# Kernel optimization log

Hardware: AMD Instinct MI355X
Metric: run time of the kernel (lower is better)

Reference implementation:

```python
import jax, jax.numpy as jnp
import numpy as np

HIDDEN = 2048
N_HEADS = 16
HEAD_DIM = HIDDEN // N_HEADS  # 128
GROUP_SIZE = 128
ROPE_THETA = 10000.0
EPS = 1e-8
THRESH = 0.5


def ternary_quantize_groupwise(w):
    O, I = w.shape
    wg = w.reshape(O, I // GROUP_SIZE, GROUP_SIZE)
    scale = jnp.maximum(jnp.mean(jnp.abs(wg), axis=-1, keepdims=True), EPS)
    wn = wg / scale
    q = jnp.where(wn > THRESH, 1.0, jnp.where(wn < -THRESH, -1.0, 0.0))
    return (q * scale).reshape(O, I)


def quantize_with_ste(w):
    wq = ternary_quantize_groupwise(w)
    return w + jax.lax.stop_gradient(wq - w)


def rope_tables(seqlen):
    half = HEAD_DIM // 2
    inv_freq = 1.0 / (ROPE_THETA ** (jnp.arange(half, dtype=jnp.float32) / half))
    freqs = jnp.arange(seqlen, dtype=jnp.float32)[:, None] * inv_freq[None, :]  # [S, half]
    return jnp.cos(freqs), jnp.sin(freqs)


def apply_rope(x, cos, sin):
    # x: [B, H, S, D]; cos/sin: [S, D/2]
    d = x.shape[-1]
    x1, x2 = x[..., : d // 2], x[..., d // 2:]
    c = cos[None, None, :, :].astype(x.dtype)
    s = sin[None, None, :, :].astype(x.dtype)
    return jnp.concatenate([x1 * c - x2 * s, x1 * s + x2 * c], axis=-1)


def setup_inputs() -> dict:
    key = jax.random.key(0)
    ks = jax.random.split(key, 5)
    B, S = 1, 2048
    hidden_states = jax.random.normal(ks[0], (B, S, HIDDEN), dtype=jnp.float32)
    attention_mask = jnp.ones((B, S), dtype=jnp.int32)
    init_scale = 1.0 / np.sqrt(HIDDEN)
    wq = jax.random.normal(ks[1], (HIDDEN, HIDDEN), dtype=jnp.float32) * init_scale
    wk = jax.random.normal(ks[2], (HIDDEN, HIDDEN), dtype=jnp.float32) * init_scale
    wv = jax.random.normal(ks[3], (HIDDEN, HIDDEN), dtype=jnp.float32) * init_scale
    wo = jax.random.normal(ks[4], (HIDDEN, HIDDEN), dtype=jnp.float32) * init_scale
    return {"hidden_states": hidden_states, "attention_mask": attention_mask,
            "wq": wq, "wk": wk, "wv": wv, "wo": wo}


def reference(hidden_states, attention_mask, wq, wk, wv, wo):
    B, S, _ = hidden_states.shape
    cos, sin = rope_tables(S)

    def proj(x, w):
        w_q = quantize_with_ste(w)
        y = jnp.einsum('bsi,oi->bso', x, w_q)
        return y.reshape(B, S, N_HEADS, HEAD_DIM).transpose(0, 2, 1, 3)  # [B,H,S,D]

    q = apply_rope(proj(hidden_states, wq), cos, sin)
    k = apply_rope(proj(hidden_states, wk), cos, sin)
    v = proj(hidden_states, wv)

    scores = jnp.einsum('bhsd,bhtd->bhst', q, k) / np.sqrt(HEAD_DIM)
    causal = jnp.triu(jnp.ones((S, S), dtype=bool), k=1)
    scores = jnp.where(causal[None, None, :, :], -jnp.inf, scores)
    pad = (attention_mask == 0)[:, None, None, :]
    scores = jnp.where(pad, -jnp.inf, scores)

    probs = jax.nn.softmax(scores, axis=-1)
    out = jnp.einsum('bhst,bhtd->bhsd', probs, v)
    out = out.transpose(0, 2, 1, 3).reshape(B, S, HIDDEN)

    wo_q = quantize_with_ste(wo)
    return jnp.einsum('bso,po->bsp', out, wo_q)
```

## Files before the change

### kernel.cpp

```cpp
#include <hip/hip_runtime.h>
#include <cstdint>
#include <cstddef>


typedef __attribute__((ext_vector_type(8))) short bf16x8;
typedef __attribute__((ext_vector_type(4))) float f32x4;
typedef __attribute__((address_space(3))) void lds_void;
typedef const __attribute__((address_space(1))) void gmem_void;

__device__ __forceinline__ short f2bf(float x) {
    union { float f; uint32_t u; } c; c.f = x;
    uint32_t r = (c.u + 0x7FFFu + ((c.u >> 16) & 1u)) >> 16;
    return (short)r;
}
__device__ __forceinline__ float bf2f(short x) {
    union { uint32_t u; float f; } c; c.u = ((uint32_t)(uint16_t)x) << 16;
    return c.f;
}

__global__ __launch_bounds__(64) void zero_flag(int* f) {
    if (threadIdx.x == 0) *f = 0;
}

__global__ __launch_bounds__(256) void detect_kernel(
    const unsigned short* __restrict__ p, int n, int* __restrict__ flag)
{
    int tid = blockIdx.x * 256 + threadIdx.x;
    int cnt = 0;
    for (int i = tid; i < n; i += 65536) {
        int e = (p[i] >> 7) & 0xFF;
        cnt += (e >= 0xF0) ? 1 : 0;
    }
#pragma unroll
    for (int off = 1; off < 64; off <<= 1) cnt += __shfl_xor(cnt, off);
    if ((threadIdx.x & 63) == 0 && cnt) atomicAdd(flag, cnt);
}

__global__ __launch_bounds__(256) void convert_kernel(
    const void* __restrict__ in, short* __restrict__ out, int n,
    const int* __restrict__ flag)
{
    bool isf32 = (*flag > 1000);
    int i = (blockIdx.x * 256 + threadIdx.x) * 4;
    if (i >= n) return;
    if (isf32) {
        float4 v = *(const float4*)((const float*)in + i);
        short4 o;
        o.x = f2bf(v.x); o.y = f2bf(v.y); o.z = f2bf(v.z); o.w = f2bf(v.w);
        *(short4*)(out + i) = o;
    } else {
        *(short4*)(out + i) = *(const short4*)((const short*)in + i);
    }
}

__global__ __launch_bounds__(256) void quant_kernel(
    const void* __restrict__ w0, const void* __restrict__ w1,
    const void* __restrict__ w2, const void* __restrict__ w3,
    short* __restrict__ q0, short* __restrict__ q1,
    short* __restrict__ q2, short* __restrict__ q3,
    const int* __restrict__ flag)
{
    bool isf32 = (*flag > 1000);
    int t   = blockIdx.x * 256 + threadIdx.x;
    int mat = t >> 20;
    int e4  = t & 1048575;
    const void* w = (mat == 0) ? w0 : (mat == 1) ? w1 : (mat == 2) ? w2 : w3;
    short*      q = (mat == 0) ? q0 : (mat == 1) ? q1 : (mat == 2) ? q2 : q3;
    float a0, a1, a2, a3;
    if (isf32) {
        float4 v = *(const float4*)((const float*)w + (long long)e4 * 4);
        a0 = v.x; a1 = v.y; a2 = v.z; a3 = v.w;
    } else {
        short4 v = *(const short4*)((const short*)w + (long long)e4 * 4);
        a0 = bf2f(v.x); a1 = bf2f(v.y); a2 = bf2f(v.z); a3 = bf2f(v.w);
    }
    float s = fabsf(a0) + fabsf(a1) + fabsf(a2) + fabsf(a3);
#pragma unroll
    for (int off = 1; off < 32; off <<= 1) s += __shfl_xor(s, off);
    float scale = fmaxf(s * (1.0f / 128.0f), 1e-8f);
    float inv = 1.0f / scale;
    auto qz = [&](float a) -> short {
        float na = a * inv;
        return f2bf((na > 0.5f) ? scale : (na < -0.5f) ? -scale : 0.0f);
    };
    short4 o;
    o.x = qz(a0); o.y = qz(a1); o.z = qz(a2); o.w = qz(a3);
    *(short4*)(q + (long long)e4 * 4) = o;
}

__global__ __launch_bounds__(256, 2) void gemm_qkv(
    const short* __restrict__ A, const short* __restrict__ B,
    short* __restrict__ C)
{
    __shared__ short lds[30720];

    int wg = blockIdx.y * 32 + blockIdx.x;
    int sw = (wg & 7) * 64 + (wg >> 3);
    int bx = sw & 31, by = sw >> 5;

    const short* Ab = A + (long long)by * 128 * 2048;
    const short* Bb = B + (long long)bx * 192 * 2048;

    int tid = threadIdx.x, lane = tid & 63, wid = tid >> 6;
    int wr = wid >> 1, wc = wid & 1;
    int quad = lane >> 4, lm = lane & 15;

    f32x4 acc[4][6];
#pragma unroll
    for (int i = 0; i < 4; i++)
#pragma unroll
        for (int j = 0; j < 6; j++)
#pragma unroll
            for (int r = 0; r < 4; r++) acc[i][j][r] = 0.0f;

    auto stage = [&](int tn, short* buf) {
        short* dA = buf;
        short* dB = buf + 4096;
#pragma unroll
        for (int l = 0; l < 2; l++) {
            int ci  = l * 256 + tid;
            int row = ci >> 2;
            int kc  = ((ci & 3) - (row >> 1)) & 3;
            const short* gp = Ab + (long long)row * 2048 + tn * 32 + kc * 8;
            __builtin_amdgcn_global_load_lds((gmem_void*)gp, (lds_void*)(dA + ci * 8), 16, 0, 0);
        }
#pragma unroll
        for (int l = 0; l < 3; l++) {
            int ci  = l * 256 + tid;
            int row = ci >> 2;
            int kc  = ((ci & 3) - (row >> 1)) & 3;
            const short* gp = Bb + (long long)row * 2048 + tn * 32 + kc * 8;
            __builtin_amdgcn_global_load_lds((gmem_void*)gp, (lds_void*)(dB + ci * 8), 16, 0, 0);
        }
    };

    auto tile = [&](short* cur, short* nxt, int tn, bool pf) {
        if (pf) stage(tn, nxt);
        short* cA = cur;
        short* cB = cur + 4096;
        bf16x8 af[4], bg[6];
#pragma unroll
        for (int m = 0; m < 4; m++) {
            int R = wr * 64 + m * 16 + lm;
            af[m] = *(const bf16x8*)(cA + R * 32 + (((quad + (R >> 1)) & 3) << 3));
        }
#pragma unroll
        for (int n = 0; n < 3; n++) {
            int R = wc * 96 + n * 16 + lm;
            bg[n] = *(const bf16x8*)(cB + R * 32 + (((quad + (R >> 1)) & 3) << 3));
        }
        __builtin_amdgcn_s_setprio(1);
#pragma unroll
        for (int m = 0; m < 4; m++)
#pragma unroll
            for (int n = 0; n < 3; n++)
                acc[m][n] = __builtin_amdgcn_mfma_f32_16x16x32_bf16(af[m], bg[n], acc[m][n], 0, 0, 0);
        __builtin_amdgcn_s_setprio(0);
#pragma unroll
        for (int n = 3; n < 6; n++) {
            int R = wc * 96 + n * 16 + lm;
            bg[n] = *(const bf16x8*)(cB + R * 32 + (((quad + (R >> 1)) & 3) << 3));
        }
        __builtin_amdgcn_s_setprio(1);
#pragma unroll
        for (int m = 0; m < 4; m++)
#pragma unroll
            for (int n = 3; n < 6; n++)
                acc[m][n] = __builtin_amdgcn_mfma_f32_16x16x32_bf16(af[m], bg[n], acc[m][n], 0, 0, 0);
        __builtin_amdgcn_s_setprio(0);
        if (pf) asm volatile("s_waitcnt vmcnt(5)" ::: "memory");
        else    asm volatile("s_waitcnt vmcnt(0)" ::: "memory");
        __builtin_amdgcn_s_barrier();
    };

    short* c0 = lds;
    short* c1 = lds + 10240;
    short* c2 = lds + 20480;
    stage(0, c0);
    stage(1, c1);
    asm volatile("s_waitcnt vmcnt(5)" ::: "memory");
    __builtin_amdgcn_s_barrier();

    for (int t = 0; t < 64; t++) {
        tile(c0, c2, t + 2, t + 2 < 64);
        short* tmp = c0; c0 = c1; c1 = c2; c2 = tmp;
    }

#pragma unroll
    for (int m = 0; m < 4; m++)
#pragma unroll
        for (int n = 0; n < 6; n++)
#pragma unroll
            for (int r = 0; r < 4; r++) {
                int row = by * 128 + wr * 64 + m * 16 + quad * 4 + r;
                int col = bx * 192 + wc * 96 + n * 16 + lm;
                C[(long long)row * 6144 + col] = f2bf(acc[m][n][r]);
            }
}

__global__ __launch_bounds__(256) void vtrans_kernel(
    const short* __restrict__ qkv, short* __restrict__ v_t)
{
    __shared__ short lt[4096];
    int bt = blockIdx.x, bo = blockIdx.y;
    int tid = threadIdx.x;
    int r = tid >> 3, c = tid & 7;
#pragma unroll
    for (int h = 0; h < 2; h++) {
        int row = h * 32 + r;
        bf16x8 v = *(const bf16x8*)(qkv + (long long)(bt * 64 + row) * 6144 + 4096 + bo * 64 + c * 8);
        *(bf16x8*)(lt + row * 64 + ((c ^ (row & 7)) << 3)) = v;
    }
    __syncthreads();
#pragma unroll
    for (int h = 0; h < 2; h++) {
        int o = h * 32 + r;
        bf16x8 ov;
#pragma unroll
        for (int k = 0; k < 8; k++) {
            int row = c * 8 + k;
            ov[k] = lt[row * 64 + ((((o >> 3) ^ (row & 7))) << 3) + (o & 7)];
        }
        *(bf16x8*)(v_t + (long long)(bo * 64 + o) * 2048 + bt * 64 + c * 8) = ov;
    }
}

__global__ __launch_bounds__(256, 2) void gemm_wo(
    const short* __restrict__ A, const short* __restrict__ B,
    float* __restrict__ C)
{
    __shared__ short lds[18432];

    int wg = blockIdx.y * 32 + blockIdx.x;
    int sw = (wg & 7) * 64 + (wg >> 3);
    int bx = sw & 31, by = sw >> 5;

    const short* Ab = A + (long long)by * 128 * 2048;
    const short* Bb = B + (long long)bx * 64 * 2048;

    int tid = threadIdx.x, lane = tid & 63, wid = tid >> 6;
    int wr = wid >> 1, wc = wid & 1;
    int quad = lane >> 4, lm = lane & 15;

    f32x4 acc[4][2];
#pragma unroll
    for (int i = 0; i < 4; i++)
#pragma unroll
        for (int j = 0; j < 2; j++)
#pragma unroll
            for (int r = 0; r < 4; r++) acc[i][j][r] = 0.0f;

    auto stage = [&](int tn, short* buf) {
        short* dA = buf;
        short* dB = buf + 4096;
#pragma unroll
        for (int l = 0; l < 2; l++) {
            int ci  = l * 256 + tid;
            int row = ci >> 2;
            int kc  = ((ci & 3) - (row >> 1)) & 3;
            const short* gp = Ab + (long long)row * 2048 + tn * 32 + kc * 8;
            __builtin_amdgcn_global_load_lds((gmem_void*)gp, (lds_void*)(dA + ci * 8), 16, 0, 0);
        }
        {
            int ci  = tid;
            int row = ci >> 2;
            int kc  = ((ci & 3) - (row >> 1)) & 3;
            const short* gp = Bb + (long long)row * 2048 + tn * 32 + kc * 8;
            __builtin_amdgcn_global_load_lds((gmem_void*)gp, (lds_void*)(dB + ci * 8), 16, 0, 0);
        }
    };

    auto tile = [&](short* cur, short* nxt, int tn, bool pf) {
        if (pf) stage(tn, nxt);
        short* cA = cur;
        short* cB = cur + 4096;
        bf16x8 af[4], bg[2];
#pragma unroll
        for (int m = 0; m < 4; m++) {
            int R = wr * 64 + m * 16 + lm;
            af[m] = *(const bf16x8*)(cA + R * 32 + (((quad + (R >> 1)) & 3) << 3));
        }
#pragma unroll
        for (int n = 0; n < 2; n++) {
            int R = wc * 32 + n * 16 + lm;
            bg[n] = *(const bf16x8*)(cB + R * 32 + (((quad + (R >> 1)) & 3) << 3));
        }
        __builtin_amdgcn_s_setprio(1);
#pragma unroll
        for (int m = 0; m < 4; m++)
#pragma unroll
            for (int n = 0; n < 2; n++)
                acc[m][n] = __builtin_amdgcn_mfma_f32_16x16x32_bf16(af[m], bg[n], acc[m][n], 0, 0, 0);
        __builtin_amdgcn_s_setprio(0);
        if (pf) asm volatile("s_waitcnt vmcnt(3)" ::: "memory");
        else    asm volatile("s_waitcnt vmcnt(0)" ::: "memory");
        __builtin_amdgcn_s_barrier();
    };

    short* c0 = lds;
    short* c1 = lds + 6144;
    short* c2 = lds + 12288;
    stage(0, c0);
    stage(1, c1);
    asm volatile("s_waitcnt vmcnt(3)" ::: "memory");
    __builtin_amdgcn_s_barrier();

    for (int t = 0; t < 64; t++) {
        tile(c0, c2, t + 2, t + 2 < 64);
        short* tmp = c0; c0 = c1; c1 = c2; c2 = tmp;
    }

#pragma unroll
    for (int m = 0; m < 4; m++)
#pragma unroll
        for (int n = 0; n < 2; n++)
#pragma unroll
            for (int r = 0; r < 4; r++) {
                int row = by * 128 + wr * 64 + m * 16 + quad * 4 + r;
                int col = bx * 64 + wc * 32 + n * 16 + lm;
                C[(long long)row * 2048 + col] = acc[m][n][r];
            }
}

__global__ __launch_bounds__(256) void rope_kernel(
    const short* __restrict__ qk,
    short* __restrict__ qr, short* __restrict__ kr)
{
    const float QSC = 0.1275174150637756f;
    int idx = blockIdx.x * 256 + threadIdx.x;
    int d8 = (idx & 7) * 8;
    int h  = (idx >> 3) & 15;
    int s  = idx >> 7;
    long long io = (long long)s * 6144 + h * 128 + d8;
    long long oo = (long long)h * 262144 + (long long)s * 128 + d8;
    bf16x8 x1q = *(const bf16x8*)(qk + io);
    bf16x8 x2q = *(const bf16x8*)(qk + io + 64);
    bf16x8 x1k = *(const bf16x8*)(qk + io + 2048);
    bf16x8 x2k = *(const bf16x8*)(qk + io + 2112);
    bf16x8 o1q, o2q, o1k, o2k;
#pragma unroll
    for (int j = 0; j < 8; j++) {
        float inv = exp2f((float)(d8 + j) * -0.20762050593261719f);
        float ang = (float)s * inv;
        float sn, c;
        sincosf(ang, &sn, &c);
        float a1 = bf2f(x1q[j]), a2 = bf2f(x2q[j]);
        o1q[j] = f2bf((a1 * c - a2 * sn) * QSC);
        o2q[j] = f2bf((a1 * sn + a2 * c) * QSC);
        float b1 = bf2f(x1k[j]), b2 = bf2f(x2k[j]);
        o1k[j] = f2bf(b1 * c - b2 * sn);
        o2k[j] = f2bf(b1 * sn + b2 * c);
    }
    *(bf16x8*)(qr + oo)      = o1q;
    *(bf16x8*)(qr + oo + 64) = o2q;
    *(bf16x8*)(kr + oo)      = o1k;
    *(bf16x8*)(kr + oo + 64) = o2k;
}

__global__ __launch_bounds__(256) void flash_kernel(
    const short* __restrict__ q_r, const short* __restrict__ k_r,
    const short* __restrict__ v_t, float* __restrict__ Opart,
    float* __restrict__ mpart, float* __restrict__ lpart)
{
    const float THR = 11.5f;
    int bid = blockIdx.x;
    int p = bid >> 5;
    int h = (bid >> 1) & 15;
    int z = bid & 1;

    int tid = threadIdx.x, lane = tid & 63, wv = tid >> 6;
    int quad = lane >> 4, lm = lane & 15;

    __shared__ short lK[64 * 128];
    __shared__ short lV[128 * 64];
    __shared__ short lP[64 * 64];

    const short* kb = k_r + h * 262144;
    const short* vb = v_t + h * 128 * 2048;

    for (int leg = 0; leg < 2; leg++) {
        int qt = leg ? p : 31 - p;
        int n  = qt + 1;
        int jhalf = (n + 1) >> 1;
        int jb = z ? jhalf : 0;
        int je = z ? n : jhalf;

        const short* qb = q_r + h * 262144 + (qt * 64 + wv * 16) * 128;
        bf16x8 aq[4];
#pragma unroll
        for (int kc = 0; kc < 4; kc++)
            aq[kc] = *(const bf16x8*)(qb + lm * 128 + kc * 32 + quad * 8);

        f32x4 ao[8];
#pragma unroll
        for (int nt = 0; nt < 8; nt++)
#pragma unroll
            for (int r = 0; r < 4; r++) ao[nt][r] = 0.0f;
        float mrow[4], lrow[4];
#pragma unroll
        for (int r = 0; r < 4; r++) { mrow[r] = -1e30f; lrow[r] = 0.0f; }

        if (jb < je) {
#pragma unroll
            for (int i = 0; i < 4; i++) {
                int ci = i * 256 + tid;
                int r = ci >> 4, cp = ci & 15;
                int c = (cp & 8) | ((cp & 7) ^ (r & 7));
                const short* gp = kb + (jb * 64 + r) * 128 + c * 8;
                __builtin_amdgcn_global_load_lds((gmem_void*)gp, (lds_void*)(lK + ci * 8), 16, 0, 0);
            }
        }
        __syncthreads();

        for (int jt = jb; jt < je; jt++) {
#pragma unroll
            for (int i = 0; i < 4; i++) {
                int ci = i * 256 + tid;
                int r = ci >> 3, cp = ci & 7;
                int c = cp ^ (r & 7);
                const short* gp = vb + r * 2048 + jt * 64 + c * 8;
                __builtin_amdgcn_global_load_lds((gmem_void*)gp, (lds_void*)(lV + ci * 8), 16, 0, 0);
            }
            f32x4 as[4];
#pragma unroll
            for (int nt = 0; nt < 4; nt++)
#pragma unroll
                for (int r = 0; r < 4; r++) as[nt][r] = 0.0f;
            __builtin_amdgcn_s_setprio(1);
#pragma unroll
            for (int kc = 0; kc < 4; kc++) {
#pragma unroll
                for (int nt = 0; nt < 4; nt++) {
                    int r = nt * 16 + lm;
                    int c = kc * 4 + quad;
                    int slot = (c & 8) | ((c & 7) ^ (r & 7));
                    bf16x8 bk = *(const bf16x8*)(lK + (r * 16 + slot) * 8);
                    as[nt] = __builtin_amdgcn_mfma_f32_16x16x32_bf16(aq[kc], bk, as[nt], 0, 0, 0);
                }
            }
            __builtin_amdgcn_s_setprio(0);
            if (jt == qt) {
#pragma unroll
                for (int nt = 0; nt < 4; nt++)
#pragma unroll
                    for (int r = 0; r < 4; r++) {
                        int qg = wv * 16 + quad * 4 + r;
                        int tg = nt * 16 + lm;
                        if (tg > qg) as[nt][r] = -1e30f;
                    }
            }
#pragma unroll
            for (int r = 0; r < 4; r++) {
                float lmax = fmaxf(fmaxf(as[0][r], as[1][r]), fmaxf(as[2][r], as[3][r]));
                if (__any(lmax > mrow[r] + THR)) {
                    float mx = lmax;
#pragma unroll
                    for (int off = 1; off < 16; off <<= 1) mx = fmaxf(mx, __shfl_xor(mx, off));
                    if (mx > mrow[r] + THR) {
                        float alpha = exp2f(mrow[r] - mx);
                        lrow[r] *= alpha;
#pragma unroll
                        for (int nt = 0; nt < 8; nt++) ao[nt][r] *= alpha;
                        mrow[r] = mx;
                    }
                }
                float ps = 0.0f;
#pragma unroll
                for (int nt = 0; nt < 4; nt++) {
                    float pv = exp2f(as[nt][r] - mrow[r]);
                    as[nt][r] = pv;
                    ps += pv;
                }
                lrow[r] += ps;
                int row = wv * 16 + quad * 4 + r;
#pragma unroll
                for (int nt = 0; nt < 4; nt++) {
                    int slot = (nt * 2 + (lm >> 3) + 2 * quad) & 7;
                    lP[row * 64 + slot * 8 + (lm & 7)] = f2bf(as[nt][r]);
                }
            }
            __syncthreads();
            if (jt + 1 < je) {
#pragma unroll
                for (int i = 0; i < 4; i++) {
                    int ci = i * 256 + tid;
                    int r = ci >> 4, cp = ci & 15;
                    int c = (cp & 8) | ((cp & 7) ^ (r & 7));
                    const short* gp = kb + ((jt + 1) * 64 + r) * 128 + c * 8;
                    __builtin_amdgcn_global_load_lds((gmem_void*)gp, (lds_void*)(lK + ci * 8), 16, 0, 0);
                }
            }
            __builtin_amdgcn_s_setprio(1);
#pragma unroll
            for (int kt = 0; kt < 2; kt++) {
                int prow = wv * 16 + lm;
                int slot = (kt * 4 + quad + 2 * (lm >> 2)) & 7;
                bf16x8 ap = *(const bf16x8*)(lP + prow * 64 + slot * 8);
#pragma unroll
                for (int nt = 0; nt < 8; nt++) {
                    int r = nt * 16 + lm;
                    int c = kt * 4 + quad;
                    int vslot = c ^ (r & 7);
                    bf16x8 bv = *(const bf16x8*)(lV + (r * 8 + vslot) * 8);
                    ao[nt] = __builtin_amdgcn_mfma_f32_16x16x32_bf16(ap, bv, ao[nt], 0, 0, 0);
                }
            }
            __builtin_amdgcn_s_setprio(0);
            __syncthreads();
        }

        float* Ob = Opart + (long long)z * 4194304;
#pragma unroll
        for (int r = 0; r < 4; r++) {
            float l = lrow[r];
#pragma unroll
            for (int off = 1; off < 16; off <<= 1) l += __shfl_xor(l, off);
            int sg = qt * 64 + wv * 16 + quad * 4 + r;
#pragma unroll
            for (int nt = 0; nt < 8; nt++) {
                int dg = h * 128 + nt * 16 + lm;
                Ob[(long long)sg * 2048 + dg] = ao[nt][r];
            }
            if (lm == 0) {
                mpart[z * 32768 + h * 2048 + sg] = mrow[r];
                lpart[z * 32768 + h * 2048 + sg] = l;
            }
        }
    }
}

__global__ __launch_bounds__(256) void combine_kernel(
    const float* __restrict__ O0, const float* __restrict__ O1,
    const float* __restrict__ mpart, const float* __restrict__ lpart,
    short* __restrict__ attn)
{
    int idx = blockIdx.x * 256 + threadIdx.x;
    int e = idx * 4;
    int s = e >> 11, h = (e & 2047) >> 7;
    float m0 = mpart[h * 2048 + s], m1 = mpart[32768 + h * 2048 + s];
    float l0 = lpart[h * 2048 + s], l1 = lpart[32768 + h * 2048 + s];
    float M = fmaxf(m0, m1);
    float w0 = exp2f(m0 - M), w1 = exp2f(m1 - M);
    float inv = 1.0f / (l0 * w0 + l1 * w1);
    float4 a = *(const float4*)(O0 + e);
    float4 b = *(const float4*)(O1 + e);
    short4 o;
    o.x = f2bf((a.x * w0 + b.x * w1) * inv);
    o.y = f2bf((a.y * w0 + b.y * w1) * inv);
    o.z = f2bf((a.z * w0 + b.z * w1) * inv);
    o.w = f2bf((a.w * w0 + b.w * w1) * inv);
    *(short4*)(attn + e) = o;
}

extern "C" void kernel_launch(void* const* d_in, const int* in_sizes, int n_in,
                              void* d_out, int out_size, void* d_ws, size_t ws_size,
                              hipStream_t stream)
{
    const void* x  = d_in[0];
    const void* wq = d_in[2];
    const void* wk = d_in[3];
    const void* wv = d_in[4];
    const void* wo = d_in[5];

    char* ws = (char*)d_ws;
    size_t off = 0;
    auto alloc = [&](size_t b) { void* p = ws + off; off += (b + 255) & ~(size_t)255; return p; };
    short* wqkv_q = (short*)alloc(25165824);
    short* wo_q   = (short*)alloc(8388608);
    float* Opart  = (float*)alloc(33554432);
    short* qkv    = (short*)Opart;
    short* v_t    = (short*)alloc(8388608);
    short* q_r    = (short*)alloc(8388608);
    short* k_r    = (short*)alloc(8388608);
    short* attn   = (short*)alloc(8388608);
    short* x_bf   = (short*)alloc(8388608);
    float* mpart  = (float*)alloc(262144);
    float* lpart  = (float*)alloc(262144);
    int*   flag   = (int*)alloc(256);
    if (off > ws_size) return;

    zero_flag<<<1, 64, 0, stream>>>(flag);
    detect_kernel<<<256, 256, 0, stream>>>(
        (const unsigned short*)x, in_sizes[0], flag);
    convert_kernel<<<4096, 256, 0, stream>>>(x, x_bf, 4194304, flag);

    quant_kernel<<<16384, 256, 0, stream>>>(wq, wk, wv, wo,
        wqkv_q, wqkv_q + 4194304, wqkv_q + 8388608, wo_q, flag);

    gemm_qkv<<<dim3(32, 16), 256, 0, stream>>>(x_bf, wqkv_q, qkv);

    rope_kernel<<<1024, 256, 0, stream>>>(qkv, q_r, k_r);
    vtrans_kernel<<<dim3(32, 32), 256, 0, stream>>>(qkv, v_t);

    flash_kernel<<<512, 256, 0, stream>>>(q_r, k_r, v_t, Opart, mpart, lpart);
    combine_kernel<<<4096, 256, 0, stream>>>(
        Opart, Opart + 4194304, mpart, lpart, attn);

    gemm_wo<<<dim3(32, 16), 256, 0, stream>>>(attn, wo_q, (float*)d_out);
}
```

Measured before the change: 306.1 us.

## Split flash attention KV range four ways and merge partials

Flash attention now splits each query tile's KV range into four chunks instead of two, doubling the grid to 1024 blocks, and sets a minimum occupancy of 4 blocks per CU. The combine kernel merges four partial outputs, skipping chunks that are empty. Partial buffers reuse dead workspace regions (the quantized QKV weights and the bf16 x scratch) to avoid extra allocation. The aim is better CU utilisation on the MI355X. In exchange it adds more partial-output write and read traffic, a heavier combine step, and register pressure from the occupancy bound.

```diff
diff --git a/kernel.cpp b/kernel.cpp
--- a/kernel.cpp
+++ b/kernel.cpp
@@ -357,16 +357,18 @@
     *(bf16x8*)(kr + oo + 64) = o2k;
 }
 
-__global__ __launch_bounds__(256) void flash_kernel(
+__global__ __launch_bounds__(256, 4) void flash_kernel(
     const short* __restrict__ q_r, const short* __restrict__ k_r,
-    const short* __restrict__ v_t, float* __restrict__ Opart,
+    const short* __restrict__ v_t,
+    float* __restrict__ O0, float* __restrict__ O1,
+    float* __restrict__ O2, float* __restrict__ O3,
     float* __restrict__ mpart, float* __restrict__ lpart)
 {
     const float THR = 11.5f;
     int bid = blockIdx.x;
-    int p = bid >> 5;
-    int h = (bid >> 1) & 15;
-    int z = bid & 1;
+    int zq = bid & 3;
+    int h  = (bid >> 2) & 15;
+    int p  = bid >> 6;
 
     int tid = threadIdx.x, lane = tid & 63, wv = tid >> 6;
     int quad = lane >> 4, lm = lane & 15;
@@ -377,13 +379,13 @@
 
     const short* kb = k_r + h * 262144;
     const short* vb = v_t + h * 128 * 2048;
+    float* Ob = (zq == 0) ? O0 : (zq == 1) ? O1 : (zq == 2) ? O2 : O3;
 
     for (int leg = 0; leg < 2; leg++) {
         int qt = leg ? p : 31 - p;
         int n  = qt + 1;
-        int jhalf = (n + 1) >> 1;
-        int jb = z ? jhalf : 0;
-        int je = z ? n : jhalf;
+        int jb = (n * zq) >> 2;
+        int je = (n * (zq + 1)) >> 2;
 
         const short* qb = q_r + h * 262144 + (qt * 64 + wv * 16) * 128;
         bf16x8 aq[4];
@@ -509,21 +511,22 @@
             __syncthreads();
         }
 
-        float* Ob = Opart + (long long)z * 4194304;
 #pragma unroll
         for (int r = 0; r < 4; r++) {
             float l = lrow[r];
 #pragma unroll
             for (int off = 1; off < 16; off <<= 1) l += __shfl_xor(l, off);
             int sg = qt * 64 + wv * 16 + quad * 4 + r;
-#pragma unroll
-            for (int nt = 0; nt < 8; nt++) {
-                int dg = h * 128 + nt * 16 + lm;
-                Ob[(long long)sg * 2048 + dg] = ao[nt][r];
+            if (jb < je) {
+#pragma unroll
+                for (int nt = 0; nt < 8; nt++) {
+                    int dg = h * 128 + nt * 16 + lm;
+                    Ob[(long long)sg * 2048 + dg] = ao[nt][r];
+                }
             }
             if (lm == 0) {
-                mpart[z * 32768 + h * 2048 + sg] = mrow[r];
-                lpart[z * 32768 + h * 2048 + sg] = l;
+                mpart[zq * 32768 + h * 2048 + sg] = mrow[r];
+                lpart[zq * 32768 + h * 2048 + sg] = l;
             }
         }
     }
@@ -531,24 +534,37 @@
 
 __global__ __launch_bounds__(256) void combine_kernel(
     const float* __restrict__ O0, const float* __restrict__ O1,
+    const float* __restrict__ O2, const float* __restrict__ O3,
     const float* __restrict__ mpart, const float* __restrict__ lpart,
     short* __restrict__ attn)
 {
     int idx = blockIdx.x * 256 + threadIdx.x;
     int e = idx * 4;
     int s = e >> 11, h = (e & 2047) >> 7;
-    float m0 = mpart[h * 2048 + s], m1 = mpart[32768 + h * 2048 + s];
-    float l0 = lpart[h * 2048 + s], l1 = lpart[32768 + h * 2048 + s];
-    float M = fmaxf(m0, m1);
-    float w0 = exp2f(m0 - M), w1 = exp2f(m1 - M);
-    float inv = 1.0f / (l0 * w0 + l1 * w1);
-    float4 a = *(const float4*)(O0 + e);
-    float4 b = *(const float4*)(O1 + e);
+    float m[4], l[4];
+#pragma unroll
+    for (int i = 0; i < 4; i++) {
+        m[i] = mpart[i * 32768 + h * 2048 + s];
+        l[i] = lpart[i * 32768 + h * 2048 + s];
+    }
+    float M = fmaxf(fmaxf(m[0], m[1]), fmaxf(m[2], m[3]));
+    const float* Os[4] = { O0, O1, O2, O3 };
+    float den = 0.0f, ax = 0.0f, ay = 0.0f, az = 0.0f, aw = 0.0f;
+#pragma unroll
+    for (int i = 0; i < 4; i++) {
+        if (l[i] > 0.0f) {
+            float w = exp2f(m[i] - M);
+            float4 a = *(const float4*)(Os[i] + e);
+            ax += a.x * w; ay += a.y * w; az += a.z * w; aw += a.w * w;
+            den += l[i] * w;
+        }
+    }
+    float inv = 1.0f / den;
     short4 o;
-    o.x = f2bf((a.x * w0 + b.x * w1) * inv);
-    o.y = f2bf((a.y * w0 + b.y * w1) * inv);
-    o.z = f2bf((a.z * w0 + b.z * w1) * inv);
-    o.w = f2bf((a.w * w0 + b.w * w1) * inv);
+    o.x = f2bf(ax * inv);
+    o.y = f2bf(ay * inv);
+    o.z = f2bf(az * inv);
+    o.w = f2bf(aw * inv);
     *(short4*)(attn + e) = o;
 }
 
@@ -567,17 +583,23 @@
     auto alloc = [&](size_t b) { void* p = ws + off; off += (b + 255) & ~(size_t)255; return p; };
     short* wqkv_q = (short*)alloc(25165824);
     short* wo_q   = (short*)alloc(8388608);
-    float* Opart  = (float*)alloc(33554432);
-    short* qkv    = (short*)Opart;
+    float* Op01   = (float*)alloc(33554432);
+    short* qkv    = (short*)Op01;
     short* v_t    = (short*)alloc(8388608);
     short* q_r    = (short*)alloc(8388608);
     short* k_r    = (short*)alloc(8388608);
-    short* attn   = (short*)alloc(8388608);
-    short* x_bf   = (short*)alloc(8388608);
-    float* mpart  = (float*)alloc(262144);
-    float* lpart  = (float*)alloc(262144);
+    char*  scr16  = (char*)alloc(16777216);
+    short* x_bf   = (short*)scr16;
+    float* mpart  = (float*)alloc(524288);
+    float* lpart  = (float*)alloc(524288);
     int*   flag   = (int*)alloc(256);
     if (off > ws_size) return;
+
+    float* O0 = Op01;
+    float* O1 = Op01 + 4194304;
+    float* O2 = (float*)wqkv_q;
+    float* O3 = (float*)scr16;
+    short* attn = (short*)((char*)wqkv_q + 16777216);
 
     zero_flag<<<1, 64, 0, stream>>>(flag);
     detect_kernel<<<256, 256, 0, stream>>>(
@@ -592,9 +614,10 @@
     rope_kernel<<<1024, 256, 0, stream>>>(qkv, q_r, k_r);
     vtrans_kernel<<<dim3(32, 32), 256, 0, stream>>>(qkv, v_t);
 
-    flash_kernel<<<512, 256, 0, stream>>>(q_r, k_r, v_t, Opart, mpart, lpart);
+    flash_kernel<<<1024, 256, 0, stream>>>(q_r, k_r, v_t,
+        O0, O1, O2, O3, mpart, lpart);
     combine_kernel<<<4096, 256, 0, stream>>>(
-        Opart, Opart + 4194304, mpart, lpart, attn);
+        O0, O1, O2, O3, mpart, lpart, attn);
 
     gemm_wo<<<dim3(32, 16), 256, 0, stream>>>(attn, wo_q, (float*)d_out);
 }
```

Result: no change. 309.3 us (+1.0%).
